# Performance work log

Measured on AMD Instinct MI355X. Metric: run time of the kernel, lower is better.

Reference implementation:

```python
import jax, jax.numpy as jnp
import numpy as np

N, E, G = 200000, 600000, 1024
NF_IN, EF_IN, H = 32, 16, 512
BN_EPS = 1e-5


def _bn(x, gamma, beta):
    # eval-mode BatchNorm1d with running_mean=0, running_var=1
    return x * (gamma / jnp.sqrt(1.0 + BN_EPS)) + beta


def setup_inputs() -> dict:
    key = jax.random.key(0)
    ks = jax.random.split(key, 32)
    s = 0.05
    inp = {
        'nf': jax.random.normal(ks[0], (N, NF_IN), jnp.float32),
        'ef': jax.random.normal(ks[1], (E, EF_IN), jnp.float32),
        'gf': jax.random.normal(ks[2], (G, H), jnp.float32),
        'device_params': jax.random.uniform(ks[3], (N,), jnp.float32),
        'node_y': jax.random.randint(ks[4], (N,), 0, 9),
        'batch_idx': jnp.sort(jax.random.randint(ks[5], (N,), 0, G)),
        'edge_index': jax.random.randint(ks[6], (2, E), 0, N),
        'nf_w1': jax.random.normal(ks[7], (NF_IN + 9, H), jnp.float32) * s,
        'nf_b1': jax.random.normal(ks[8], (H,), jnp.float32) * s,
        'nf_g1': jax.random.uniform(ks[9], (H,), jnp.float32, 0.5, 1.5),
        'nf_be1': jax.random.normal(ks[10], (H,), jnp.float32) * s,
        'nf_w2': jax.random.normal(ks[11], (H, H), jnp.float32) * s,
        'nf_b2': jax.random.normal(ks[12], (H,), jnp.float32) * s,
        'ef_w1': jax.random.normal(ks[13], (EF_IN, H), jnp.float32) * s,
        'ef_b1': jax.random.normal(ks[14], (H,), jnp.float32) * s,
        'ef_g1': jax.random.uniform(ks[15], (H,), jnp.float32, 0.5, 1.5),
        'ef_be1': jax.random.normal(ks[16], (H,), jnp.float32) * s,
        'ef_w2': jax.random.normal(ks[17], (H, H), jnp.float32) * s,
        'ef_b2': jax.random.normal(ks[18], (H,), jnp.float32) * s,
        'ow1': jax.random.normal(ks[19], (H, H), jnp.float32) * s,
        'ob1': jax.random.normal(ks[20], (H,), jnp.float32) * s,
        'og1': jax.random.uniform(ks[21], (H,), jnp.float32, 0.5, 1.5),
        'obe1': jax.random.normal(ks[22], (H,), jnp.float32) * s,
        'ow2': jax.random.normal(ks[23], (H, H), jnp.float32) * s,
        'ob2': jax.random.normal(ks[24], (H,), jnp.float32) * s,
        'og2': jax.random.uniform(ks[25], (H,), jnp.float32, 0.5, 1.5),
        'obe2': jax.random.normal(ks[26], (H,), jnp.float32) * s,
        'ow3': jax.random.normal(ks[27], (H, 2), jnp.float32) * s,
        'ob3': jax.random.normal(ks[28], (2,), jnp.float32) * s,
    }
    return inp


def reference(nf, ef, gf, device_params, node_y, batch_idx, edge_index,
              nf_w1, nf_b1, nf_g1, nf_be1, nf_w2, nf_b2,
              ef_w1, ef_b1, ef_g1, ef_be1, ef_w2, ef_b2,
              ow1, ob1, og1, obe1, ow2, ob2, og2, obe2, ow3, ob3):
    num_graphs = gf.shape[0]
    gelu = lambda x: jax.nn.gelu(x, approximate=False)  # torch nn.GELU default

    # DeviceParam_MLP: augment node features with scaled one-hot of node class
    nf_aug = jnp.concatenate(
        [nf, jax.nn.one_hot(node_y, 9, dtype=nf.dtype) * device_params[:, None]],
        axis=-1)  # [N, nf_in+9]
    h_n = gelu(_bn(nf_aug @ nf_w1 + nf_b1, nf_g1, nf_be1)) @ nf_w2 + nf_b2  # [N,H]
    h_e = gelu(_bn(ef @ ef_w1 + ef_b1, ef_g1, ef_be1)) @ ef_w2 + ef_b2      # [E,H]

    # two scatter_add pools into graph features
    gh = gf
    gh = gh + jax.ops.segment_sum(h_n, batch_idx, num_segments=num_graphs)
    edge_graph = batch_idx[edge_index[0]]  # graph id of each edge's source node
    gh = gh + jax.ops.segment_sum(h_e, edge_graph, num_segments=num_graphs)

    # output MLP (layer_num=3): two hidden blocks + final Linear -> 2
    x = gelu(_bn(gh @ ow1 + ob1, og1, obe1))
    x = gelu(_bn(x @ ow2 + ob2, og2, obe2))
    return x @ ow3 + ob3  # [G, 2]
```

## Files before the change

kernel.cpp:

```cpp
#include <hip/hip_runtime.h>
#include <hip/hip_bf16.h>

#define NN 200000
#define NE 600000
#define NG 1024
#define HH 512

typedef short short8 __attribute__((ext_vector_type(8)));
typedef float f32x4 __attribute__((ext_vector_type(4)));

__device__ __forceinline__ unsigned short f2bf(float f){
  unsigned u = __float_as_uint(f);
  u += 0x7fffu + ((u >> 16) & 1u);
  return (unsigned short)(u >> 16);
}
__device__ __forceinline__ float bf2f(unsigned short h){
  return __uint_as_float(((unsigned)h) << 16);
}

__device__ __forceinline__ short8 cvt8pk(float4 a, float4 b){
  union { short8 s; __hip_bfloat162 h[4]; } u;
  u.h[0] = __float22bfloat162_rn(make_float2(a.x, a.y));
  u.h[1] = __float22bfloat162_rn(make_float2(a.z, a.w));
  u.h[2] = __float22bfloat162_rn(make_float2(b.x, b.y));
  u.h[3] = __float22bfloat162_rn(make_float2(b.z, b.w));
  return u.s;
}

__device__ __forceinline__ void split8(const float* v, short8* hi, short8* lo){
  union { short8 s; __hip_bfloat162 h[4]; unsigned u[4]; } H, L;
#pragma unroll
  for (int p=0;p<4;++p){
    float a = v[2*p], b = v[2*p+1];
    H.h[p] = __float22bfloat162_rn(make_float2(a, b));
    unsigned hu = H.u[p];
    L.h[p] = __float22bfloat162_rn(make_float2(a - __uint_as_float(hu << 16),
                                               b - __uint_as_float(hu & 0xffff0000u)));
  }
  *hi = H.s; *lo = L.s;
}

__device__ __forceinline__ float gelu_f(float x){
  float p = __builtin_fmaf(x*x, -0.10294325f, -2.3022085f);
  float e = __builtin_amdgcn_exp2f(x * p);
  return x * __builtin_amdgcn_rcpf(1.0f + e);
}

__global__ __launch_bounds__(256) void kpre(
    const float* __restrict__ nfw1, const float* __restrict__ nfb1,
    const float* __restrict__ nfg1, const float* __restrict__ nfbe1,
    const float* __restrict__ efw1, const float* __restrict__ efb1,
    const float* __restrict__ efg1, const float* __restrict__ efbe1,
    unsigned short* __restrict__ w1nT, unsigned short* __restrict__ w1eT,
    float* __restrict__ b1n, float* __restrict__ b1e,
    const int* __restrict__ bidx, int* __restrict__ nstart,
    const int* __restrict__ eidx, int* __restrict__ eg, int* __restrict__ hpart){
  __shared__ int h[NG];
  const float rs = 0.99999500003750f;
  int b = blockIdx.x, t = threadIdx.x;
  if (b < 196){
    int tid = b*256 + t;
    if (tid < 512*64){
      int c = tid >> 6, k = tid & 63;
      float w = (k < 41) ? nfw1[k*HH + c] * nfg1[c] * rs : 0.0f;
      w1nT[tid] = f2bf(w);
    } else if (tid < 512*96){
      int u = tid - 512*64; int c = u >> 5, k = u & 31;
      float w = (k < 16) ? efw1[k*HH + c] * efg1[c] * rs : 0.0f;
      w1eT[u] = f2bf(w);
    } else if (tid < 512*96 + 512){
      int c = tid - 512*96;
      b1n[c] = nfb1[c]*nfg1[c]*rs + nfbe1[c];
    } else if (tid < 512*96 + 1024){
      int c = tid - (512*96 + 512);
      b1e[c] = efb1[c]*efg1[c]*rs + efbe1[c];
    }
  } else if (b < 978){
    int i = (b-196)*256 + t;
    if (i < NN){
      int g0 = bidx[i];
      int g1 = (i+1 < NN) ? bidx[i+1] : NG;
      for (int g = g0+1; g <= g1; ++g) nstart[g] = i+1;
      if (i == 0) for (int g = 0; g <= g0; ++g) nstart[g] = 0;
    }
  } else {
    int hb = b - 978;
    for (int u = t; u < NG; u += 256) h[u] = 0;
    __syncthreads();
    const int per = (NE + 255) / 256;
    const int lo = hb*per, hi = min(lo + per, NE);
    for (int e = lo + t; e < hi; e += 256){
      int g = bidx[eidx[e]];
      eg[e] = g;
      atomicAdd(&h[g], 1);
    }
    __syncthreads();
    for (int u = t; u < NG; u += 256) hpart[hb*NG + u] = h[u];
  }
}

__global__ __launch_bounds__(1024) void kscat(const int* __restrict__ eg,
    const int* __restrict__ hpart, int* __restrict__ estart, int* __restrict__ perm,
    const int* __restrict__ nstart, const float* __restrict__ gf,
    const float* __restrict__ b2n, const float* __restrict__ b2e, float* __restrict__ gh){
  __shared__ int s[NG];
  __shared__ int h[NG];
  __shared__ int base[NG];
  const int b = blockIdx.x, t = threadIdx.x;
  int T = 0, P = 0;
  for (int hb = 0; hb < 256; ++hb){
    int hp = hpart[hb*NG + t];
    T += hp;
    if (hb < b) P += hp;
  }
  s[t] = T; __syncthreads();
  for (int d = 1; d < NG; d <<= 1){
    int x = (t >= d) ? s[t-d] : 0;
    __syncthreads();
    s[t] += x;
    __syncthreads();
  }
  const int excl = s[t] - T;
  base[t] = excl + P;
  h[t] = 0;
  if (b == 0){
    estart[t] = excl;
    if (t == NG-1) estart[NG] = s[t];
  }
  __syncthreads();
  const int per = (NE + 255) / 256;
  const int lo = b*per, hi = min(lo + per, NE);
  for (int e = lo + t; e < hi; e += 1024){
    int g = eg[e];
    int p = base[g] + atomicAdd(&h[g], 1);
    perm[p] = e;
  }
  if (t < 512){
    int i = b*512 + t;
    int f = i*4;
    int r = f >> 9, c = f & 511;
    float cn = (float)(nstart[r+1] - nstart[r]);
    float ce = (float)(s[r] - ((r > 0) ? s[r-1] : 0));
    float4 gv = *(const float4*)&gf[f];
    float4 bn4 = *(const float4*)&b2n[c];
    float4 be4 = *(const float4*)&b2e[c];
    float4 o;
    o.x = gv.x + cn*bn4.x + ce*be4.x;
    o.y = gv.y + cn*bn4.y + ce*be4.y;
    o.z = gv.z + cn*bn4.z + ce*be4.z;
    o.w = gv.w + cn*bn4.w + ce*be4.w;
    *(float4*)&gh[f] = o;
  }
}

__global__ __launch_bounds__(256) void kmain(
    const float* __restrict__ nf, const float* __restrict__ dp, const int* __restrict__ ny,
    const int* __restrict__ nstart, const float* __restrict__ ef, const int* __restrict__ perm,
    const int* __restrict__ estart, const unsigned short* __restrict__ w1nT,
    const unsigned short* __restrict__ w1eT, const float* __restrict__ b1n,
    const float* __restrict__ b1e, float* __restrict__ S){
  const int t = threadIdx.x;
  const int lane = t & 63, w = t >> 6;
  const int q = lane >> 4, m = lane & 15;
  const short8 zz = {0,0,0,0,0,0,0,0};
  if (blockIdx.x < 2048){
    const int g = blockIdx.x >> 1;
    const int c0 = ((blockIdx.x & 1) << 8) + (w << 6);
    short8 bfr[4]; float bias[4]; float colacc[4] = {0.f,0.f,0.f,0.f};
#pragma unroll
    for (int nt=0; nt<4; ++nt){
      int c = c0 + (nt<<4) + m;
      bfr[nt] = *(const short8*)(w1eT + (c << 5) + (q << 3));
      bias[nt] = b1e[c];
    }
    const int s0 = estart[g], s1 = estart[g+1];
    const int nfull = (s1 - s0) >> 4;
    int rb = s0;
    for (int ch=0; ch<nfull; ++ch, rb += 16){
      int e = perm[rb + m];
      short8 f = zz;
      if (q < 2){
        const float4* ap = (const float4*)(ef + (size_t)e*16 + (q<<3));
        f = cvt8pk(ap[0], ap[1]);
      }
#pragma unroll
      for (int nt=0; nt<4; ++nt){
        f32x4 acc = {bias[nt], bias[nt], bias[nt], bias[nt]};
        acc = __builtin_amdgcn_mfma_f32_16x16x32_bf16(f, bfr[nt], acc, 0, 0, 0);
        colacc[nt] += (gelu_f(acc[0]) + gelu_f(acc[1])) + (gelu_f(acc[2]) + gelu_f(acc[3]));
      }
    }
    if (rb < s1){
      int row = rb + m;
      int e = perm[(row < s1) ? row : s0];
      short8 f = zz;
      if (q < 2){
        const float4* ap = (const float4*)(ef + (size_t)e*16 + (q<<3));
        f = cvt8pk(ap[0], ap[1]);
      }
      const int vr = s1 - rb;
#pragma unroll
      for (int nt=0; nt<4; ++nt){
        f32x4 acc = {bias[nt], bias[nt], bias[nt], bias[nt]};
        acc = __builtin_amdgcn_mfma_f32_16x16x32_bf16(f, bfr[nt], acc, 0, 0, 0);
        float v0 = (q*4+0 < vr) ? gelu_f(acc[0]) : 0.f;
        float v1 = (q*4+1 < vr) ? gelu_f(acc[1]) : 0.f;
        float v2 = (q*4+2 < vr) ? gelu_f(acc[2]) : 0.f;
        float v3 = (q*4+3 < vr) ? gelu_f(acc[3]) : 0.f;
        colacc[nt] += (v0+v1)+(v2+v3);
      }
    }
#pragma unroll
    for (int nt=0; nt<4; ++nt){
      float s = colacc[nt];
      s += __shfl_xor(s, 16); s += __shfl_xor(s, 32);
      if (lane < 16) S[(size_t)g*1024 + 512 + c0 + (nt<<4) + lane] = s;
    }
  } else {
    const int b2 = blockIdx.x - 2048;
    const int g = b2 >> 2;
    const int c0 = ((b2 & 3) << 7) + (w << 5);
    short8 bf0[2], bf1[2]; float bias[2]; float colacc[2] = {0.f,0.f};
#pragma unroll
    for (int nt=0; nt<2; ++nt){
      int c = c0 + (nt<<4) + m;
      const short8* bp = (const short8*)(w1nT + (c << 6) + (q << 3));
      bf0[nt] = bp[0]; bf1[nt] = bp[4];
      bias[nt] = b1n[c];
    }
    const int s0 = nstart[g], s1 = nstart[g+1];
    const int nfull = (s1 - s0) >> 4;
    int rb = s0;
    for (int ch=0; ch<nfull; ++ch, rb += 16){
      int ar = rb + m;
      const float4* ap = (const float4*)(nf + (size_t)ar*32 + (q<<3));
      short8 f = cvt8pk(ap[0], ap[1]);
      int cls = ny[ar];
      short dpb = (short)f2bf(dp[ar]);
      short8 h = zz;
      if (q == 0){
#pragma unroll
        for (int j=0;j<8;++j) h[j] = (cls==j) ? dpb : (short)0;
      } else if (q == 1 && cls == 8) h[0] = dpb;
#pragma unroll
      for (int nt=0; nt<2; ++nt){
        f32x4 acc = {bias[nt], bias[nt], bias[nt], bias[nt]};
        acc = __builtin_amdgcn_mfma_f32_16x16x32_bf16(f, bf0[nt], acc, 0, 0, 0);
        acc = __builtin_amdgcn_mfma_f32_16x16x32_bf16(h, bf1[nt], acc, 0, 0, 0);
        colacc[nt] += (gelu_f(acc[0]) + gelu_f(acc[1])) + (gelu_f(acc[2]) + gelu_f(acc[3]));
      }
    }
    if (rb < s1){
      int row = rb + m;
      int ar = (row < s1) ? row : s0;
      const float4* ap = (const float4*)(nf + (size_t)ar*32 + (q<<3));
      short8 f = cvt8pk(ap[0], ap[1]);
      int cls = ny[ar];
      short dpb = (short)f2bf(dp[ar]);
      short8 h = zz;
      if (q == 0){
#pragma unroll
        for (int j=0;j<8;++j) h[j] = (cls==j) ? dpb : (short)0;
      } else if (q == 1 && cls == 8) h[0] = dpb;
      const int vr = s1 - rb;
#pragma unroll
      for (int nt=0; nt<2; ++nt){
        f32x4 acc = {bias[nt], bias[nt], bias[nt], bias[nt]};
        acc = __builtin_amdgcn_mfma_f32_16x16x32_bf16(f, bf0[nt], acc, 0, 0, 0);
        acc = __builtin_amdgcn_mfma_f32_16x16x32_bf16(h, bf1[nt], acc, 0, 0, 0);
        float v0 = (q*4+0 < vr) ? gelu_f(acc[0]) : 0.f;
        float v1 = (q*4+1 < vr) ? gelu_f(acc[1]) : 0.f;
        float v2 = (q*4+2 < vr) ? gelu_f(acc[2]) : 0.f;
        float v3 = (q*4+3 < vr) ? gelu_f(acc[3]) : 0.f;
        colacc[nt] += (v0+v1)+(v2+v3);
      }
    }
#pragma unroll
    for (int nt=0; nt<2; ++nt){
      float s = colacc[nt];
      s += __shfl_xor(s, 16); s += __shfl_xor(s, 32);
      if (lane < 16) S[(size_t)g*1024 + c0 + (nt<<4) + lane] = s;
    }
  }
}

__global__ __launch_bounds__(256) void kgemm3(const float* __restrict__ A, int lda, int nkc,
    const float* __restrict__ B0, const float* __restrict__ B1,
    float* __restrict__ out, const float* __restrict__ pre, const float* __restrict__ bias,
    const float* __restrict__ gam, const float* __restrict__ bet){
  const int t = threadIdx.x, lane = t & 63, w = t >> 6;
  const int q = lane >> 4, m = lane & 15;
  const int c0 = blockIdx.x*32, r0 = blockIdx.y*64 + w*16;
  f32x4 acc[2] = {{0.f,0.f,0.f,0.f},{0.f,0.f,0.f,0.f}};
  const float* ap = A + (size_t)(r0 + m)*lda + (q<<3);
  for (int kc = 0; kc < nkc; ++kc){
    const int ko = kc*32;
    float4 x = *(const float4*)(ap + ko);
    float4 y = *(const float4*)(ap + ko + 4);
    float v[8] = {x.x,x.y,x.z,x.w,y.x,y.y,y.z,y.w};
    short8 ah, al;
    split8(v, &ah, &al);
    const float* Bp = (kc < 16) ? B0 : B1;
    const float* bp = Bp + (size_t)((kc & 15)*32 + (q<<3))*HH + c0 + m;
#pragma unroll
    for (int cf=0; cf<2; ++cf){
      float bv[8];
#pragma unroll
      for (int j=0;j<8;++j) bv[j] = bp[(size_t)j*HH + cf*16];
      short8 bh, bl;
      split8(bv, &bh, &bl);
      acc[cf] = __builtin_amdgcn_mfma_f32_16x16x32_bf16(ah, bh, acc[cf], 0, 0, 0);
      acc[cf] = __builtin_amdgcn_mfma_f32_16x16x32_bf16(ah, bl, acc[cf], 0, 0, 0);
      acc[cf] = __builtin_amdgcn_mfma_f32_16x16x32_bf16(al, bh, acc[cf], 0, 0, 0);
    }
  }
  const float rs = 0.99999500003750f;
#pragma unroll
  for (int cf=0; cf<2; ++cf){
    int c = c0 + cf*16 + m;
    float sc = 0.f, bi = 0.f, be = 0.f;
    if (!pre){ sc = gam[c]*rs; bi = bias[c]; be = bet[c]; }
#pragma unroll
    for (int i=0;i<4;++i){
      int r = blockIdx.y*64 + w*16 + q*4 + i;
      float vv = acc[cf][i];
      if (pre) vv += pre[(size_t)r*HH + c];
      else vv = gelu_f((vv + bi)*sc + be);
      out[(size_t)r*HH + c] = vv;
    }
  }
}

__global__ __launch_bounds__(256) void kfinal(const float* __restrict__ x2, const float* __restrict__ w3,
    const float* __restrict__ b3, float* __restrict__ out){
  const int lane = threadIdx.x & 63, wv = threadIdx.x >> 6;
  const int r = blockIdx.x*4 + wv;
  float a0 = 0.f, a1 = 0.f;
#pragma unroll
  for (int tt=0; tt<8; ++tt){
    int k = lane + tt*64;
    float x = x2[(size_t)r*HH + k];
    a0 = __builtin_fmaf(x, w3[2*k], a0);
    a1 = __builtin_fmaf(x, w3[2*k+1], a1);
  }
#pragma unroll
  for (int d=1; d<64; d<<=1){ a0 += __shfl_xor(a0, d); a1 += __shfl_xor(a1, d); }
  if (lane == 0){ out[r*2] = a0 + b3[0]; out[r*2+1] = a1 + b3[1]; }
}

extern "C" void kernel_launch(void* const* d_in, const int* in_sizes, int n_in,
                              void* d_out, int out_size, void* d_ws, size_t ws_size,
                              hipStream_t stream) {
  const float* nf    = (const float*)d_in[0];
  const float* ef    = (const float*)d_in[1];
  const float* gf    = (const float*)d_in[2];
  const float* dp    = (const float*)d_in[3];
  const int*   ny    = (const int*)d_in[4];
  const int*   bidx  = (const int*)d_in[5];
  const int*   eidx  = (const int*)d_in[6];
  const float* nfw1  = (const float*)d_in[7];
  const float* nfb1  = (const float*)d_in[8];
  const float* nfg1  = (const float*)d_in[9];
  const float* nfbe1 = (const float*)d_in[10];
  const float* w2n   = (const float*)d_in[11];
  const float* b2n   = (const float*)d_in[12];
  const float* efw1  = (const float*)d_in[13];
  const float* efb1  = (const float*)d_in[14];
  const float* efg1  = (const float*)d_in[15];
  const float* efbe1 = (const float*)d_in[16];
  const float* w2e   = (const float*)d_in[17];
  const float* b2e   = (const float*)d_in[18];
  const float* ow1   = (const float*)d_in[19];
  const float* ob1   = (const float*)d_in[20];
  const float* og1   = (const float*)d_in[21];
  const float* obe1  = (const float*)d_in[22];
  const float* ow2   = (const float*)d_in[23];
  const float* ob2   = (const float*)d_in[24];
  const float* og2   = (const float*)d_in[25];
  const float* obe2  = (const float*)d_in[26];
  const float* ow3   = (const float*)d_in[27];
  const float* ob3   = (const float*)d_in[28];

  float* S    = (float*)d_ws;
  int* nstart = (int*)(S + NG*1024);
  int* estart = nstart + NG + 1;
  int* eg     = estart + NG + 1;
  int* perm   = eg + NE;
  int* hpart  = perm + NE;
  unsigned short* w1nT = (unsigned short*)(hpart + 256*NG);
  unsigned short* w1eT = w1nT + HH*64;
  float* b1n  = (float*)(w1eT + HH*32);
  float* b1e  = b1n + HH;
  float* gh   = b1e + HH;
  float* xg2  = gh + NG*HH;
  float* x2f  = xg2 + NG*HH;

  kpre<<<1234, 256, 0, stream>>>(nfw1, nfb1, nfg1, nfbe1, efw1, efb1, efg1, efbe1,
                                 w1nT, w1eT, b1n, b1e, bidx, nstart, eidx, eg, hpart);
  kscat<<<256, 1024, 0, stream>>>(eg, hpart, estart, perm, nstart, gf, b2n, b2e, gh);
  kmain<<<6144, 256, 0, stream>>>(nf, dp, ny, nstart, ef, perm, estart,
                                  w1nT, w1eT, b1n, b1e, S);
  kgemm3<<<dim3(16,16), 256, 0, stream>>>(S, 1024, 32, w2n, w2e, gh, gh,
                                          nullptr, nullptr, nullptr);
  kgemm3<<<dim3(16,16), 256, 0, stream>>>(gh, 512, 16, ow1, ow1, xg2, nullptr,
                                          ob1, og1, obe1);
  kgemm3<<<dim3(16,16), 256, 0, stream>>>(xg2, 512, 16, ow2, ow2, x2f, nullptr,
                                          ob2, og2, obe2);
  kfinal<<<NG/4, 256, 0, stream>>>(x2f, ow3, ob3, (float*)d_out);
}
```

Measured before the change: 372.0 us.

## Split-K the small GEMMs with atomics and move BN+GELU into consumer prologues

The three dense GEMMs now split the K dimension across blockIdx.z and accumulate into their outputs with unsafeAtomicAdd. This raises the block count from 256 to 512–1024 so more CUs are busy. Because partial sums can no longer apply the nonlinear epilogue, kscat pre-fills the outputs with their biases, and the BN+GELU is applied in the prologue of the next GEMM and of kfinal. The trade-off is recomputing GELU for every column block that reads a row, plus atomic traffic and nondeterministic summation order. The bias is also passed directly as the MFMA accumulator input instead of building it inside the loop.

```diff
diff --git a/kernel.cpp b/kernel.cpp
--- a/kernel.cpp
+++ b/kernel.cpp
@@ -102,7 +102,9 @@
 __global__ __launch_bounds__(1024) void kscat(const int* __restrict__ eg,
     const int* __restrict__ hpart, int* __restrict__ estart, int* __restrict__ perm,
     const int* __restrict__ nstart, const float* __restrict__ gf,
-    const float* __restrict__ b2n, const float* __restrict__ b2e, float* __restrict__ gh){
+    const float* __restrict__ b2n, const float* __restrict__ b2e, float* __restrict__ gh,
+    const float* __restrict__ ob1, const float* __restrict__ ob2,
+    float* __restrict__ y1, float* __restrict__ y2){
   __shared__ int s[NG];
   __shared__ int h[NG];
   __shared__ int base[NG];
@@ -150,6 +152,8 @@
     o.z = gv.z + cn*bn4.z + ce*be4.z;
     o.w = gv.w + cn*bn4.w + ce*be4.w;
     *(float4*)&gh[f] = o;
+    *(float4*)&y1[f] = *(const float4*)&ob1[c];
+    *(float4*)&y2[f] = *(const float4*)&ob2[c];
   }
 }
 
@@ -166,12 +170,13 @@
   if (blockIdx.x < 2048){
     const int g = blockIdx.x >> 1;
     const int c0 = ((blockIdx.x & 1) << 8) + (w << 6);
-    short8 bfr[4]; float bias[4]; float colacc[4] = {0.f,0.f,0.f,0.f};
+    short8 bfr[4]; f32x4 biasv[4]; float colacc[4] = {0.f,0.f,0.f,0.f};
 #pragma unroll
     for (int nt=0; nt<4; ++nt){
       int c = c0 + (nt<<4) + m;
       bfr[nt] = *(const short8*)(w1eT + (c << 5) + (q << 3));
-      bias[nt] = b1e[c];
+      float b = b1e[c];
+      biasv[nt][0]=b; biasv[nt][1]=b; biasv[nt][2]=b; biasv[nt][3]=b;
     }
     const int s0 = estart[g], s1 = estart[g+1];
     const int nfull = (s1 - s0) >> 4;
@@ -185,8 +190,7 @@
       }
 #pragma unroll
       for (int nt=0; nt<4; ++nt){
-        f32x4 acc = {bias[nt], bias[nt], bias[nt], bias[nt]};
-        acc = __builtin_amdgcn_mfma_f32_16x16x32_bf16(f, bfr[nt], acc, 0, 0, 0);
+        f32x4 acc = __builtin_amdgcn_mfma_f32_16x16x32_bf16(f, bfr[nt], biasv[nt], 0, 0, 0);
         colacc[nt] += (gelu_f(acc[0]) + gelu_f(acc[1])) + (gelu_f(acc[2]) + gelu_f(acc[3]));
       }
     }
@@ -201,8 +205,7 @@
       const int vr = s1 - rb;
 #pragma unroll
       for (int nt=0; nt<4; ++nt){
-        f32x4 acc = {bias[nt], bias[nt], bias[nt], bias[nt]};
-        acc = __builtin_amdgcn_mfma_f32_16x16x32_bf16(f, bfr[nt], acc, 0, 0, 0);
+        f32x4 acc = __builtin_amdgcn_mfma_f32_16x16x32_bf16(f, bfr[nt], biasv[nt], 0, 0, 0);
         float v0 = (q*4+0 < vr) ? gelu_f(acc[0]) : 0.f;
         float v1 = (q*4+1 < vr) ? gelu_f(acc[1]) : 0.f;
         float v2 = (q*4+2 < vr) ? gelu_f(acc[2]) : 0.f;
@@ -220,13 +223,14 @@
     const int b2 = blockIdx.x - 2048;
     const int g = b2 >> 2;
     const int c0 = ((b2 & 3) << 7) + (w << 5);
-    short8 bf0[2], bf1[2]; float bias[2]; float colacc[2] = {0.f,0.f};
+    short8 bf0[2], bf1[2]; f32x4 biasv[2]; float colacc[2] = {0.f,0.f};
 #pragma unroll
     for (int nt=0; nt<2; ++nt){
       int c = c0 + (nt<<4) + m;
       const short8* bp = (const short8*)(w1nT + (c << 6) + (q << 3));
       bf0[nt] = bp[0]; bf1[nt] = bp[4];
-      bias[nt] = b1n[c];
+      float b = b1n[c];
+      biasv[nt][0]=b; biasv[nt][1]=b; biasv[nt][2]=b; biasv[nt][3]=b;
     }
     const int s0 = nstart[g], s1 = nstart[g+1];
     const int nfull = (s1 - s0) >> 4;
@@ -244,8 +248,7 @@
       } else if (q == 1 && cls == 8) h[0] = dpb;
 #pragma unroll
       for (int nt=0; nt<2; ++nt){
-        f32x4 acc = {bias[nt], bias[nt], bias[nt], bias[nt]};
-        acc = __builtin_amdgcn_mfma_f32_16x16x32_bf16(f, bf0[nt], acc, 0, 0, 0);
+        f32x4 acc = __builtin_amdgcn_mfma_f32_16x16x32_bf16(f, bf0[nt], biasv[nt], 0, 0, 0);
         acc = __builtin_amdgcn_mfma_f32_16x16x32_bf16(h, bf1[nt], acc, 0, 0, 0);
         colacc[nt] += (gelu_f(acc[0]) + gelu_f(acc[1])) + (gelu_f(acc[2]) + gelu_f(acc[3]));
       }
@@ -265,8 +268,7 @@
       const int vr = s1 - rb;
 #pragma unroll
       for (int nt=0; nt<2; ++nt){
-        f32x4 acc = {bias[nt], bias[nt], bias[nt], bias[nt]};
-        acc = __builtin_amdgcn_mfma_f32_16x16x32_bf16(f, bf0[nt], acc, 0, 0, 0);
+        f32x4 acc = __builtin_amdgcn_mfma_f32_16x16x32_bf16(f, bf0[nt], biasv[nt], 0, 0, 0);
         acc = __builtin_amdgcn_mfma_f32_16x16x32_bf16(h, bf1[nt], acc, 0, 0, 0);
         float v0 = (q*4+0 < vr) ? gelu_f(acc[0]) : 0.f;
         float v1 = (q*4+1 < vr) ? gelu_f(acc[1]) : 0.f;
@@ -284,20 +286,26 @@
   }
 }
 
-__global__ __launch_bounds__(256) void kgemm3(const float* __restrict__ A, int lda, int nkc,
-    const float* __restrict__ B0, const float* __restrict__ B1,
-    float* __restrict__ out, const float* __restrict__ pre, const float* __restrict__ bias,
-    const float* __restrict__ gam, const float* __restrict__ bet){
+__global__ __launch_bounds__(256) void kgemm4(const float* __restrict__ A, int lda, int nkc,
+    const float* __restrict__ B0, const float* __restrict__ B1, float* __restrict__ out,
+    int act, const float* __restrict__ gam, const float* __restrict__ bet){
   const int t = threadIdx.x, lane = t & 63, w = t >> 6;
   const int q = lane >> 4, m = lane & 15;
   const int c0 = blockIdx.x*32, r0 = blockIdx.y*64 + w*16;
+  const int kz = blockIdx.z * nkc;
+  const float rs = 0.99999500003750f;
   f32x4 acc[2] = {{0.f,0.f,0.f,0.f},{0.f,0.f,0.f,0.f}};
   const float* ap = A + (size_t)(r0 + m)*lda + (q<<3);
-  for (int kc = 0; kc < nkc; ++kc){
+  for (int kc = kz; kc < kz + nkc; ++kc){
     const int ko = kc*32;
     float4 x = *(const float4*)(ap + ko);
     float4 y = *(const float4*)(ap + ko + 4);
     float v[8] = {x.x,x.y,x.z,x.w,y.x,y.y,y.z,y.w};
+    if (act){
+      int kb = ko + (q<<3);
+#pragma unroll
+      for (int j=0;j<8;++j) v[j] = gelu_f(v[j]*(gam[kb+j]*rs) + bet[kb+j]);
+    }
     short8 ah, al;
     split8(v, &ah, &al);
     const float* Bp = (kc < 16) ? B0 : B1;
@@ -314,32 +322,28 @@
       acc[cf] = __builtin_amdgcn_mfma_f32_16x16x32_bf16(al, bh, acc[cf], 0, 0, 0);
     }
   }
-  const float rs = 0.99999500003750f;
 #pragma unroll
   for (int cf=0; cf<2; ++cf){
     int c = c0 + cf*16 + m;
-    float sc = 0.f, bi = 0.f, be = 0.f;
-    if (!pre){ sc = gam[c]*rs; bi = bias[c]; be = bet[c]; }
 #pragma unroll
     for (int i=0;i<4;++i){
       int r = blockIdx.y*64 + w*16 + q*4 + i;
-      float vv = acc[cf][i];
-      if (pre) vv += pre[(size_t)r*HH + c];
-      else vv = gelu_f((vv + bi)*sc + be);
-      out[(size_t)r*HH + c] = vv;
-    }
-  }
-}
-
-__global__ __launch_bounds__(256) void kfinal(const float* __restrict__ x2, const float* __restrict__ w3,
-    const float* __restrict__ b3, float* __restrict__ out){
+      unsafeAtomicAdd(&out[(size_t)r*HH + c], acc[cf][i]);
+    }
+  }
+}
+
+__global__ __launch_bounds__(256) void kfinal(const float* __restrict__ y2,
+    const float* __restrict__ og2, const float* __restrict__ obe2,
+    const float* __restrict__ w3, const float* __restrict__ b3, float* __restrict__ out){
+  const float rs = 0.99999500003750f;
   const int lane = threadIdx.x & 63, wv = threadIdx.x >> 6;
   const int r = blockIdx.x*4 + wv;
   float a0 = 0.f, a1 = 0.f;
 #pragma unroll
   for (int tt=0; tt<8; ++tt){
     int k = lane + tt*64;
-    float x = x2[(size_t)r*HH + k];
+    float x = gelu_f(y2[(size_t)r*HH + k] * (og2[k]*rs) + obe2[k]);
     a0 = __builtin_fmaf(x, w3[2*k], a0);
     a1 = __builtin_fmaf(x, w3[2*k+1], a1);
   }
@@ -392,19 +396,17 @@
   float* b1n  = (float*)(w1eT + HH*32);
   float* b1e  = b1n + HH;
   float* gh   = b1e + HH;
-  float* xg2  = gh + NG*HH;
-  float* x2f  = xg2 + NG*HH;
+  float* y1   = gh + NG*HH;
+  float* y2   = y1 + NG*HH;
 
   kpre<<<1234, 256, 0, stream>>>(nfw1, nfb1, nfg1, nfbe1, efw1, efb1, efg1, efbe1,
                                  w1nT, w1eT, b1n, b1e, bidx, nstart, eidx, eg, hpart);
-  kscat<<<256, 1024, 0, stream>>>(eg, hpart, estart, perm, nstart, gf, b2n, b2e, gh);
+  kscat<<<256, 1024, 0, stream>>>(eg, hpart, estart, perm, nstart, gf, b2n, b2e, gh,
+                                  ob1, ob2, y1, y2);
   kmain<<<6144, 256, 0, stream>>>(nf, dp, ny, nstart, ef, perm, estart,
                                   w1nT, w1eT, b1n, b1e, S);
-  kgemm3<<<dim3(16,16), 256, 0, stream>>>(S, 1024, 32, w2n, w2e, gh, gh,
-                                          nullptr, nullptr, nullptr);
-  kgemm3<<<dim3(16,16), 256, 0, stream>>>(gh, 512, 16, ow1, ow1, xg2, nullptr,
-                                          ob1, og1, obe1);
-  kgemm3<<<dim3(16,16), 256, 0, stream>>>(xg2, 512, 16, ow2, ow2, x2f, nullptr,
-                                          ob2, og2, obe2);
-  kfinal<<<NG/4, 256, 0, stream>>>(x2f, ow3, ob3, (float*)d_out);
-}
+  kgemm4<<<dim3(16,16,4), 256, 0, stream>>>(S, 1024, 8, w2n, w2e, gh, 0, nullptr, nullptr);
+  kgemm4<<<dim3(16,16,2), 256, 0, stream>>>(gh, 512, 8, ow1, ow1, y1, 0, nullptr, nullptr);
+  kgemm4<<<dim3(16,16,2), 256, 0, stream>>>(y1, 512, 8, ow2, ow2, y2, 1, og1, obe1);
+  kfinal<<<NG/4, 256, 0, stream>>>(y2, og2, obe2, ow3, ob3, (float*)d_out);
+}
```

After: 375.3 us. No clear change (+0.9%).
